# Performance work log

Measured on AMD Instinct MI355X. Metric: run time of the kernel, lower is better.

The kernel has to match this reference:

```python
import jax, jax.numpy as jnp
import numpy as np
import math

B, C_IN, C_QK, H, W, NH = 1, 256, 128, 96, 96, 8
SCALE = math.sqrt(C_QK / NH)  # sqrt(planes/num_head) = 4.0
TEMP = 1.0


def conv1x1(x, w, b=None):
    # x: [B, Cin, H, W], w: [Cout, Cin] -> [B, Cout, H, W]
    y = jnp.einsum('bchw,oc->bohw', x, w)
    if b is not None:
        y = y + b[None, :, None, None]
    return y


def maxpool2x2(x):
    return jax.lax.reduce_window(x, -jnp.inf, jax.lax.max,
                                 (1, 1, 2, 2), (1, 1, 2, 2), 'VALID')


def setup_inputs() -> dict:
    key = jax.random.key(0)
    ks = jax.random.split(key, 5)
    x = jax.random.normal(ks[0], (B, C_IN, H, W), dtype=jnp.float32)
    # conv weights: init.normal_(w, 0, 0.01), zero bias; conv_value has no bias
    w_q = jax.random.normal(ks[1], (C_QK, C_IN), dtype=jnp.float32) * 0.01
    b_q = jnp.zeros((C_QK,), dtype=jnp.float32)
    w_k = jax.random.normal(ks[2], (C_QK, C_IN), dtype=jnp.float32) * 0.01
    b_k = jnp.zeros((C_QK,), dtype=jnp.float32)
    w_v = jax.random.normal(ks[3], (C_IN, C_IN), dtype=jnp.float32) * 0.01
    return {'x': x, 'w_q': w_q, 'b_q': b_q, 'w_k': w_k, 'b_k': b_k, 'w_v': w_v}


def reference(x, w_q, b_q, w_k, b_k, w_v):
    residual = x
    input_x = maxpool2x2(x)                       # [B, Cin, H/2, W/2]
    Hd, Wd = H // 2, W // 2
    Nq, Nk = H * W, Hd * Wd

    q = conv1x1(x, w_q, b_q)                      # [B, Cqk, H, W]
    k = conv1x1(input_x, w_k, b_k)                # [B, Cqk, Hd, Wd]
    v = conv1x1(input_x, w_v)                     # [B, Cin, Hd, Wd]

    dq = C_QK // NH
    dv = C_IN // NH
    q = q.reshape(B * NH, dq, Nq)
    k = k.reshape(B * NH, dq, Nk)
    v = v.reshape(B * NH, dv, Nk)

    # dot distance: scaled by sqrt(planes/num_head) and temp (nowd empty)
    sim = jnp.einsum('bdq,bdk->bqk', q, k) / (SCALE * TEMP)
    attn = jax.nn.softmax(sim, axis=2)            # softmax over keys

    # out = value @ attn^T  -> [B*NH, dv, Nq]
    out = jnp.einsum('bdk,bqk->bdq', v, attn)
    out = out.reshape(B, C_IN, H, W)
    return out + residual
```

## Files before the change

kernel.cpp:

```cpp
#include <hip/hip_runtime.h>
#include <hip/hip_bf16.h>
#include <math.h>

#define C_IN   256
#define C_QK   128
#define NH     8
#define H_     96
#define W_     96
#define NQ     (H_*W_)
#define HD     48
#define WD     48
#define NK     (HD*WD)
#define DQ     16
#define DV     32
#define NQC    (NQ/32)
#define NKC    (NK/32)
#define KQRT   (NKC/4)
#define KSTEPS (C_IN/16)
#define QS     0.3606737602222409f

typedef __attribute__((ext_vector_type(8)))  short short8v;
typedef __attribute__((ext_vector_type(16))) float f32x16;
typedef __attribute__((ext_vector_type(2)))  int   v2i;

union B8u { uint u[4]; short8v v; };

static __device__ inline uint cvtpk(float lo, float hi) {
    uint r;
    asm("v_cvt_pk_bf16_f32 %0, %1, %2" : "=v"(r) : "v"(lo), "v"(hi));
    return r;
}
static __device__ inline void lswap(uint a, uint b, uint& x, uint& y, int hi) {
#if __has_builtin(__builtin_amdgcn_permlane32_swap)
    v2i r = __builtin_amdgcn_permlane32_swap((int)a, (int)b, false, false);
    x = (uint)r.x;
    y = (uint)r.y;
#else
    uint bx = (uint)__shfl_xor((int)b, 32);
    uint ax = (uint)__shfl_xor((int)a, 32);
    x = hi ? bx : a;
    y = hi ? b : ax;
#endif
}
static __device__ inline float fexp2(float v) {
#if __has_builtin(__builtin_amdgcn_exp2f)
    return __builtin_amdgcn_exp2f(v);
#else
    return __expf(v * 0.6931471805599453f);
#endif
}

#define GQ_B 288
#define GK_B (GQ_B + 72)
#define G_ALL (GK_B + 144)

__global__ __launch_bounds__(256) void gemm_all(
    const float* __restrict__ x,
    const float* __restrict__ wq, const float* __restrict__ bq,
    const float* __restrict__ wk, const float* __restrict__ bk_,
    const float* __restrict__ wv,
    ushort* __restrict__ qpack, ushort* __restrict__ kpack, ushort* __restrict__ vpack)
{
    __shared__ ushort Bf[KSTEPS][64][8];
    const int tid = threadIdx.x, lane = tid & 63, wvi = tid >> 6;
    const int hi = lane >> 5;
    const int bid = blockIdx.x;

    {
        int c = tid & 31;
        int ko0 = (tid >> 5) * 4;
        if (bid < GQ_B) {
            int col = bid * 32 + c;
            #pragma unroll
            for (int u = 0; u < 4; ++u) {
                int ko = ko0 + u;
                const float* xp_ = x + (size_t)(8 * ko) * NQ + col;
                float f[8];
                #pragma unroll
                for (int j = 0; j < 8; ++j) f[j] = xp_[(size_t)j * NQ];
                uint4 w;
                w.x = cvtpk(f[0], f[1]); w.y = cvtpk(f[2], f[3]);
                w.z = cvtpk(f[4], f[5]); w.w = cvtpk(f[6], f[7]);
                *(uint4*)&Bf[ko >> 1][32 * (ko & 1) + c][0] = w;
            }
        } else {
            int kc = (bid < GK_B) ? (bid - GQ_B) : ((bid - GK_B) >> 1);
            int np = kc * 32 + c;
            int py = np / WD, px = np - py * WD;
            const float* base = x + (2 * py) * W_ + 2 * px;
            #pragma unroll
            for (int u = 0; u < 4; ++u) {
                int ko = ko0 + u;
                const float* xp_ = base + (size_t)(8 * ko) * NQ;
                float f[8];
                #pragma unroll
                for (int j = 0; j < 8; ++j) {
                    const float* p = xp_ + (size_t)j * NQ;
                    f[j] = fmaxf(fmaxf(p[0], p[1]), fmaxf(p[W_], p[W_ + 1]));
                }
                uint4 w;
                w.x = cvtpk(f[0], f[1]); w.y = cvtpk(f[2], f[3]);
                w.z = cvtpk(f[4], f[5]); w.w = cvtpk(f[6], f[7]);
                *(uint4*)&Bf[ko >> 1][32 * (ko & 1) + c][0] = w;
            }
        }
    }
    __syncthreads();

    f32x16 acc;
    #pragma unroll
    for (int r = 0; r < 16; ++r) acc[r] = 0.0f;

    const float* Wsrc;
    if (bid < GQ_B)      Wsrc = wq + (size_t)(wvi * 32 + (lane & 31)) * C_IN + 8 * hi;
    else if (bid < GK_B) Wsrc = wk + (size_t)(wvi * 32 + (lane & 31)) * C_IN + 8 * hi;
    else {
        int cb = ((bid - GK_B) & 1) * 4 + wvi;
        Wsrc = wv + (size_t)(cb * 32 + (lane & 31)) * C_IN + 8 * hi;
    }

    #pragma unroll
    for (int s = 0; s < KSTEPS; ++s) {
        float4 wa = *(const float4*)(Wsrc + 16 * s);
        float4 wb = *(const float4*)(Wsrc + 16 * s + 4);
        B8u af;
        af.u[0] = cvtpk(wa.x, wa.y); af.u[1] = cvtpk(wa.z, wa.w);
        af.u[2] = cvtpk(wb.x, wb.y); af.u[3] = cvtpk(wb.z, wb.w);
        short8v b = *(const short8v*)&Bf[s][lane][0];
        if (bid < GK_B)
            acc = __builtin_amdgcn_mfma_f32_32x32x16_bf16(af.v, b, acc, 0, 0, 0);
        else
            acc = __builtin_amdgcn_mfma_f32_32x32x16_bf16(b, af.v, acc, 0, 0, 0);
    }

    short8v F1, F2;
    if (bid < GQ_B) {
        int nc = bid, mb = wvi;
        #pragma unroll
        for (int r = 0; r < 16; ++r)
            acc[r] = (acc[r] + bq[mb * 32 + (r & 3) + 8 * (r >> 2) + 4 * hi]) * QS;
        {
            uint a0 = cvtpk(acc[0],  acc[1]),  a1 = cvtpk(acc[2],  acc[3]);
            uint b0 = cvtpk(acc[4],  acc[5]),  b1 = cvtpk(acc[6],  acc[7]);
            uint a2 = cvtpk(acc[8],  acc[9]),  a3 = cvtpk(acc[10], acc[11]);
            uint b2 = cvtpk(acc[12], acc[13]), b3 = cvtpk(acc[14], acc[15]);
            B8u f1, f2;
            lswap(a0, b0, f1.u[0], f1.u[2], hi);
            lswap(a1, b1, f1.u[1], f1.u[3], hi);
            lswap(a2, b2, f2.u[0], f2.u[2], hi);
            lswap(a3, b3, f2.u[1], f2.u[3], hi);
            F1 = f1.v; F2 = f2.v;
        }
        *(short8v*)&qpack[((size_t)((2 * mb)     * NQC + nc) * 64 + lane) * 8] = F1;
        *(short8v*)&qpack[((size_t)((2 * mb + 1) * NQC + nc) * 64 + lane) * 8] = F2;
    } else if (bid < GK_B) {
        int nc = bid - GQ_B, mb = wvi;
        #pragma unroll
        for (int r = 0; r < 16; ++r)
            acc[r] += bk_[mb * 32 + (r & 3) + 8 * (r >> 2) + 4 * hi];
        {
            uint a0 = cvtpk(acc[0],  acc[1]),  a1 = cvtpk(acc[2],  acc[3]);
            uint b0 = cvtpk(acc[4],  acc[5]),  b1 = cvtpk(acc[6],  acc[7]);
            uint a2 = cvtpk(acc[8],  acc[9]),  a3 = cvtpk(acc[10], acc[11]);
            uint b2 = cvtpk(acc[12], acc[13]), b3 = cvtpk(acc[14], acc[15]);
            B8u f1, f2;
            lswap(a0, b0, f1.u[0], f1.u[2], hi);
            lswap(a1, b1, f1.u[1], f1.u[3], hi);
            lswap(a2, b2, f2.u[0], f2.u[2], hi);
            lswap(a3, b3, f2.u[1], f2.u[3], hi);
            F1 = f1.v; F2 = f2.v;
        }
        *(short8v*)&kpack[((size_t)((2 * mb)     * NKC + nc) * 64 + lane) * 8] = F1;
        *(short8v*)&kpack[((size_t)((2 * mb + 1) * NKC + nc) * 64 + lane) * 8] = F2;
    } else {
        int vb = bid - GK_B;
        int kc = vb >> 1, cb = (vb & 1) * 4 + wvi;
        {
            uint a0 = cvtpk(acc[0],  acc[1]),  a1 = cvtpk(acc[2],  acc[3]);
            uint b0 = cvtpk(acc[4],  acc[5]),  b1 = cvtpk(acc[6],  acc[7]);
            uint a2 = cvtpk(acc[8],  acc[9]),  a3 = cvtpk(acc[10], acc[11]);
            uint b2 = cvtpk(acc[12], acc[13]), b3 = cvtpk(acc[14], acc[15]);
            B8u f1, f2;
            lswap(a0, b0, f1.u[0], f1.u[2], hi);
            lswap(a1, b1, f1.u[1], f1.u[3], hi);
            lswap(a2, b2, f2.u[0], f2.u[2], hi);
            lswap(a3, b3, f2.u[1], f2.u[3], hi);
            F1 = f1.v; F2 = f2.v;
        }
        *(short8v*)&vpack[((size_t)((cb * NKC + kc) * 2 + 0) * 64 + lane) * 8] = F1;
        *(short8v*)&vpack[((size_t)((cb * NKC + kc) * 2 + 1) * 64 + lane) * 8] = F2;
    }
}

#define CSTR 17

static __device__ inline void attn_step(short8v kc_, short8v qf, short8v v0c, short8v v1c,
                                        f32x16& o, float& rsA, float& rsB,
                                        const f32x16& zc, int hi) {
    f32x16 s = __builtin_amdgcn_mfma_f32_32x32x16_bf16(kc_, qf, zc, 0, 0, 0);
    {
        float e0 = fexp2(s[0]), e1 = fexp2(s[1]), e2 = fexp2(s[2]), e3 = fexp2(s[3]);
        float e4 = fexp2(s[4]), e5 = fexp2(s[5]), e6 = fexp2(s[6]), e7 = fexp2(s[7]);
        rsA += ((e0 + e1) + (e2 + e3)) + ((e4 + e5) + (e6 + e7));
        uint a0 = cvtpk(e0, e1), a1 = cvtpk(e2, e3);
        uint b0 = cvtpk(e4, e5), b1 = cvtpk(e6, e7);
        B8u B1;
        lswap(a0, b0, B1.u[0], B1.u[2], hi);
        lswap(a1, b1, B1.u[1], B1.u[3], hi);
        o = __builtin_amdgcn_mfma_f32_32x32x16_bf16(v0c, B1.v, o, 0, 0, 0);
    }
    {
        float e0 = fexp2(s[8]),  e1 = fexp2(s[9]),  e2 = fexp2(s[10]), e3 = fexp2(s[11]);
        float e4 = fexp2(s[12]), e5 = fexp2(s[13]), e6 = fexp2(s[14]), e7 = fexp2(s[15]);
        rsB += ((e0 + e1) + (e2 + e3)) + ((e4 + e5) + (e6 + e7));
        uint a0 = cvtpk(e0, e1), a1 = cvtpk(e2, e3);
        uint b0 = cvtpk(e4, e5), b1 = cvtpk(e6, e7);
        B8u B2;
        lswap(a0, b0, B2.u[0], B2.u[2], hi);
        lswap(a1, b1, B2.u[1], B2.u[3], hi);
        o = __builtin_amdgcn_mfma_f32_32x32x16_bf16(v1c, B2.v, o, 0, 0, 0);
    }
}

__global__ __launch_bounds__(256) void attn_kernel(const ushort* __restrict__ qpack,
                                                   const ushort* __restrict__ kpack,
                                                   const ushort* __restrict__ vpack,
                                                   const float* __restrict__ x,
                                                   float* __restrict__ out) {
    __shared__ float part[4][64][CSTR];
    const int h = blockIdx.y, qc = blockIdx.x;
    const int tid = threadIdx.x, lane = tid & 63;
    const int kh = tid >> 6;
    const int q31 = lane & 31, hi = lane >> 5;

    short8v qf = *(const short8v*)&qpack[((size_t)(h * NQC + qc) * 64 + lane) * 8];

    const char* kp = (const char*)(kpack + ((size_t)(h * NKC + kh * KQRT) * 64 + lane) * 8);
    const char* vp = (const char*)(vpack + ((size_t)(h * NKC + kh * KQRT) * 2 * 64 + lane) * 8);

    short8v kf  = *(const short8v*)kp;
    short8v v0f = *(const short8v*)vp;
    short8v v1f = *(const short8v*)(vp + 1024);

    f32x16 o, zc;
    #pragma unroll
    for (int r = 0; r < 16; ++r) { o[r] = 0.0f; zc[r] = 0.0f; }
    float rsA = 0.0f, rsB = 0.0f;

    #pragma unroll 2
    for (int c = 0; c < KQRT - 1; ++c) {
        kp += 1024; vp += 2048;
        short8v kn  = *(const short8v*)kp;
        short8v v0n = *(const short8v*)vp;
        short8v v1n = *(const short8v*)(vp + 1024);
        attn_step(kf, qf, v0f, v1f, o, rsA, rsB, zc, hi);
        kf = kn; v0f = v0n; v1f = v1n;
    }
    attn_step(kf, qf, v0f, v1f, o, rsA, rsB, zc, hi);

    float rs = rsA + rsB;
    rs += __shfl_xor(rs, 32);

    {
        float* pw = &part[kh][lane][0];
        #pragma unroll
        for (int r = 0; r < 16; ++r) pw[r] = o[r];
        pw[16] = rs;
    }
    __syncthreads();

    float rsAll = part[0][lane][16] + part[1][lane][16]
                + part[2][lane][16] + part[3][lane][16];
    float inv = 1.0f / rsAll;
    int q = qc * 32 + q31;
    #pragma unroll
    for (int i = 0; i < 4; ++i) {
        int r = 4 * kh + i;
        float val = part[0][lane][r] + part[1][lane][r]
                  + part[2][lane][r] + part[3][lane][r];
        int dv = i + 8 * kh + 4 * hi;
        size_t i0 = (size_t)(h * DV + dv) * NQ + q;
        out[i0] = val * inv + x[i0];
    }
}

extern "C" void kernel_launch(void* const* d_in, const int* in_sizes, int n_in,
                              void* d_out, int out_size, void* d_ws, size_t ws_size,
                              hipStream_t stream) {
    const float* x  = (const float*)d_in[0];
    const float* wq = (const float*)d_in[1];
    const float* bq = (const float*)d_in[2];
    const float* wk = (const float*)d_in[3];
    const float* bk = (const float*)d_in[4];
    const float* wv = (const float*)d_in[5];
    float* out = (float*)d_out;

    ushort* p = (ushort*)d_ws;
    ushort* qpack = p;  p += (size_t)NH * NQC * 64 * 8;
    ushort* kpack = p;  p += (size_t)NH * NKC * 64 * 8;
    ushort* vpack = p;  p += (size_t)NH * NKC * 2 * 64 * 8;

    gemm_all<<<G_ALL, 256, 0, stream>>>(x, wq, bq, wk, bk, wv, qpack, kpack, vpack);
    attn_kernel<<<dim3(NQC, NH), 256, 0, stream>>>(qpack, kpack, vpack, x, out);
}
```

Baseline: 111.9 us.

## Split projection GEMM K-dimension across wave pairs and double block count

The QKV projection kernel now launches twice as many blocks. Each block covers half the output channels, and its four waves form two pairs that each take half of the 256-wide reduction. Partial accumulators from the upper-K wave go through shared memory and are summed by the lower-K wave before the bias, scale and pack epilogue. The aim is more parallelism and a shorter serial MFMA chain per wave on the small projection GEMMs. The cost is that each block now reloads and converts the input x tile for half the work, plus an extra barrier and a shared-memory reduction.

```diff
diff --git a/kernel.cpp b/kernel.cpp
--- a/kernel.cpp
+++ b/kernel.cpp
@@ -49,10 +49,22 @@
     return __expf(v * 0.6931471805599453f);
 #endif
 }
-
-#define GQ_B 288
-#define GK_B (GQ_B + 72)
-#define G_ALL (GK_B + 144)
+static __device__ inline void xform(const f32x16& acc, int hi, short8v& F1, short8v& F2) {
+    uint a0 = cvtpk(acc[0],  acc[1]),  a1 = cvtpk(acc[2],  acc[3]);
+    uint b0 = cvtpk(acc[4],  acc[5]),  b1 = cvtpk(acc[6],  acc[7]);
+    uint a2 = cvtpk(acc[8],  acc[9]),  a3 = cvtpk(acc[10], acc[11]);
+    uint b2 = cvtpk(acc[12], acc[13]), b3 = cvtpk(acc[14], acc[15]);
+    B8u f1, f2;
+    lswap(a0, b0, f1.u[0], f1.u[2], hi);
+    lswap(a1, b1, f1.u[1], f1.u[3], hi);
+    lswap(a2, b2, f2.u[0], f2.u[2], hi);
+    lswap(a3, b3, f2.u[1], f2.u[3], hi);
+    F1 = f1.v; F2 = f2.v;
+}
+
+#define GQ_B 576
+#define GK_B (GQ_B + 144)
+#define G_ALL (GK_B + 288)
 
 __global__ __launch_bounds__(256) void gemm_all(
     const float* __restrict__ x,
@@ -62,15 +74,18 @@
     ushort* __restrict__ qpack, ushort* __restrict__ kpack, ushort* __restrict__ vpack)
 {
     __shared__ ushort Bf[KSTEPS][64][8];
+    __shared__ float prt[2][64][17];
     const int tid = threadIdx.x, lane = tid & 63, wvi = tid >> 6;
     const int hi = lane >> 5;
+    const int tib = wvi >> 1;
+    const int kh  = wvi & 1;
     const int bid = blockIdx.x;
 
     {
         int c = tid & 31;
         int ko0 = (tid >> 5) * 4;
         if (bid < GQ_B) {
-            int col = bid * 32 + c;
+            int col = (bid >> 1) * 32 + c;
             #pragma unroll
             for (int u = 0; u < 4; ++u) {
                 int ko = ko0 + u;
@@ -84,7 +99,7 @@
                 *(uint4*)&Bf[ko >> 1][32 * (ko & 1) + c][0] = w;
             }
         } else {
-            int kc = (bid < GK_B) ? (bid - GQ_B) : ((bid - GK_B) >> 1);
+            int kc = (bid < GK_B) ? ((bid - GQ_B) >> 1) : ((bid - GK_B) >> 2);
             int np = kc * 32 + c;
             int py = np / WD, px = np - py * WD;
             const float* base = x + (2 * py) * W_ + 2 * px;
@@ -112,15 +127,20 @@
     for (int r = 0; r < 16; ++r) acc[r] = 0.0f;
 
     const float* Wsrc;
-    if (bid < GQ_B)      Wsrc = wq + (size_t)(wvi * 32 + (lane & 31)) * C_IN + 8 * hi;
-    else if (bid < GK_B) Wsrc = wk + (size_t)(wvi * 32 + (lane & 31)) * C_IN + 8 * hi;
-    else {
-        int cb = ((bid - GK_B) & 1) * 4 + wvi;
+    if (bid < GQ_B) {
+        int mb = (bid & 1) * 2 + tib;
+        Wsrc = wq + (size_t)(mb * 32 + (lane & 31)) * C_IN + 8 * hi;
+    } else if (bid < GK_B) {
+        int mb = ((bid - GQ_B) & 1) * 2 + tib;
+        Wsrc = wk + (size_t)(mb * 32 + (lane & 31)) * C_IN + 8 * hi;
+    } else {
+        int cb = ((bid - GK_B) & 3) * 2 + tib;
         Wsrc = wv + (size_t)(cb * 32 + (lane & 31)) * C_IN + 8 * hi;
     }
 
     #pragma unroll
-    for (int s = 0; s < KSTEPS; ++s) {
+    for (int ss = 0; ss < 8; ++ss) {
+        int s = 8 * kh + ss;
         float4 wa = *(const float4*)(Wsrc + 16 * s);
         float4 wb = *(const float4*)(Wsrc + 16 * s + 4);
         B8u af;
@@ -133,62 +153,40 @@
             acc = __builtin_amdgcn_mfma_f32_32x32x16_bf16(b, af.v, acc, 0, 0, 0);
     }
 
-    short8v F1, F2;
-    if (bid < GQ_B) {
-        int nc = bid, mb = wvi;
+    if (kh == 1) {
+        float* pw = &prt[tib][lane][0];
         #pragma unroll
-        for (int r = 0; r < 16; ++r)
-            acc[r] = (acc[r] + bq[mb * 32 + (r & 3) + 8 * (r >> 2) + 4 * hi]) * QS;
-        {
-            uint a0 = cvtpk(acc[0],  acc[1]),  a1 = cvtpk(acc[2],  acc[3]);
-            uint b0 = cvtpk(acc[4],  acc[5]),  b1 = cvtpk(acc[6],  acc[7]);
-            uint a2 = cvtpk(acc[8],  acc[9]),  a3 = cvtpk(acc[10], acc[11]);
-            uint b2 = cvtpk(acc[12], acc[13]), b3 = cvtpk(acc[14], acc[15]);
-            B8u f1, f2;
-            lswap(a0, b0, f1.u[0], f1.u[2], hi);
-            lswap(a1, b1, f1.u[1], f1.u[3], hi);
-            lswap(a2, b2, f2.u[0], f2.u[2], hi);
-            lswap(a3, b3, f2.u[1], f2.u[3], hi);
-            F1 = f1.v; F2 = f2.v;
+        for (int r = 0; r < 16; ++r) pw[r] = acc[r];
+    }
+    __syncthreads();
+    if (kh == 0) {
+        const float* pw = &prt[tib][lane][0];
+        #pragma unroll
+        for (int r = 0; r < 16; ++r) acc[r] += pw[r];
+
+        short8v F1, F2;
+        if (bid < GQ_B) {
+            int nc = bid >> 1, mb = (bid & 1) * 2 + tib;
+            #pragma unroll
+            for (int r = 0; r < 16; ++r)
+                acc[r] = (acc[r] + bq[mb * 32 + (r & 3) + 8 * (r >> 2) + 4 * hi]) * QS;
+            xform(acc, hi, F1, F2);
+            *(short8v*)&qpack[((size_t)((2 * mb)     * NQC + nc) * 64 + lane) * 8] = F1;
+            *(short8v*)&qpack[((size_t)((2 * mb + 1) * NQC + nc) * 64 + lane) * 8] = F2;
+        } else if (bid < GK_B) {
+            int nc = (bid - GQ_B) >> 1, mb = ((bid - GQ_B) & 1) * 2 + tib;
+            #pragma unroll
+            for (int r = 0; r < 16; ++r)
+                acc[r] += bk_[mb * 32 + (r & 3) + 8 * (r >> 2) + 4 * hi];
+            xform(acc, hi, F1, F2);
+            *(short8v*)&kpack[((size_t)((2 * mb)     * NKC + nc) * 64 + lane) * 8] = F1;
+            *(short8v*)&kpack[((size_t)((2 * mb + 1) * NKC + nc) * 64 + lane) * 8] = F2;
+        } else {
+            int kc = (bid - GK_B) >> 2, cb = ((bid - GK_B) & 3) * 2 + tib;
+            xform(acc, hi, F1, F2);
+            *(short8v*)&vpack[((size_t)((cb * NKC + kc) * 2 + 0) * 64 + lane) * 8] = F1;
+            *(short8v*)&vpack[((size_t)((cb * NKC + kc) * 2 + 1) * 64 + lane) * 8] = F2;
         }
-        *(short8v*)&qpack[((size_t)((2 * mb)     * NQC + nc) * 64 + lane) * 8] = F1;
-        *(short8v*)&qpack[((size_t)((2 * mb + 1) * NQC + nc) * 64 + lane) * 8] = F2;
-    } else if (bid < GK_B) {
-        int nc = bid - GQ_B, mb = wvi;
-        #pragma unroll
-        for (int r = 0; r < 16; ++r)
-            acc[r] += bk_[mb * 32 + (r & 3) + 8 * (r >> 2) + 4 * hi];
-        {
-            uint a0 = cvtpk(acc[0],  acc[1]),  a1 = cvtpk(acc[2],  acc[3]);
-            uint b0 = cvtpk(acc[4],  acc[5]),  b1 = cvtpk(acc[6],  acc[7]);
-            uint a2 = cvtpk(acc[8],  acc[9]),  a3 = cvtpk(acc[10], acc[11]);
-            uint b2 = cvtpk(acc[12], acc[13]), b3 = cvtpk(acc[14], acc[15]);
-            B8u f1, f2;
-            lswap(a0, b0, f1.u[0], f1.u[2], hi);
-            lswap(a1, b1, f1.u[1], f1.u[3], hi);
-            lswap(a2, b2, f2.u[0], f2.u[2], hi);
-            lswap(a3, b3, f2.u[1], f2.u[3], hi);
-            F1 = f1.v; F2 = f2.v;
-        }
-        *(short8v*)&kpack[((size_t)((2 * mb)     * NKC + nc) * 64 + lane) * 8] = F1;
-        *(short8v*)&kpack[((size_t)((2 * mb + 1) * NKC + nc) * 64 + lane) * 8] = F2;
-    } else {
-        int vb = bid - GK_B;
-        int kc = vb >> 1, cb = (vb & 1) * 4 + wvi;
-        {
-            uint a0 = cvtpk(acc[0],  acc[1]),  a1 = cvtpk(acc[2],  acc[3]);
-            uint b0 = cvtpk(acc[4],  acc[5]),  b1 = cvtpk(acc[6],  acc[7]);
-            uint a2 = cvtpk(acc[8],  acc[9]),  a3 = cvtpk(acc[10], acc[11]);
-            uint b2 = cvtpk(acc[12], acc[13]), b3 = cvtpk(acc[14], acc[15]);
-            B8u f1, f2;
-            lswap(a0, b0, f1.u[0], f1.u[2], hi);
-            lswap(a1, b1, f1.u[1], f1.u[3], hi);
-            lswap(a2, b2, f2.u[0], f2.u[2], hi);
-            lswap(a3, b3, f2.u[1], f2.u[3], hi);
-            F1 = f1.v; F2 = f2.v;
-        }
-        *(short8v*)&vpack[((size_t)((cb * NKC + kc) * 2 + 0) * 64 + lane) * 8] = F1;
-        *(short8v*)&vpack[((size_t)((cb * NKC + kc) * 2 + 1) * 64 + lane) * 8] = F2;
     }
 }
 
```

Result: no change. 113.6 us (+1.5%).
